# Performance work log

Hardware: AMD Instinct MI355X
Metric: run time of the kernel (lower is better)

## Reference

```python
import jax, jax.numpy as jnp
import numpy as np

D_MODEL = 1024
N_HEADS = 16
HEAD_DIM = D_MODEL // N_HEADS
B, T = 4, 2048
EPS = 1e-5


def _layernorm(x, w, b):
    mu = jnp.mean(x, axis=-1, keepdims=True)
    var = jnp.mean(jnp.square(x - mu), axis=-1, keepdims=True)
    return (x - mu) * jax.lax.rsqrt(var + EPS) * w + b


def _heads(x, w, b):
    # x: [B,T,D]; w stored [in,out] so y = x @ w + b (== torch Linear)
    y = x @ w + b
    return y.reshape(B, T, N_HEADS, HEAD_DIM).transpose(0, 2, 1, 3)  # [B,H,T,hd]


def _attention(q, k, v):
    scores = jnp.einsum('bhqd,bhkd->bhqk', q, k) / np.sqrt(HEAD_DIM).astype(np.float32)
    attn = jax.nn.softmax(scores, axis=-1)  # dropout is identity in eval mode
    o = jnp.einsum('bhqk,bhkd->bhqd', attn, v)
    return o.transpose(0, 2, 1, 3).reshape(B, T, D_MODEL)


def setup_inputs() -> dict:
    key = jax.random.key(0)
    ks = jax.random.split(key, 16)
    s = 1.0 / np.sqrt(D_MODEL)
    def lin(k, din, dout):
        kw, kb = jax.random.split(k)
        return (jax.random.uniform(kw, (din, dout), jnp.float32, -s, s),
                jax.random.uniform(kb, (dout,), jnp.float32, -s, s))
    inp = {}
    inp['temporal_tokens'] = jax.random.normal(ks[0], (B, T, D_MODEL), jnp.float32)
    inp['feature_tokens'] = jax.random.normal(ks[1], (B, T, D_MODEL), jnp.float32)
    names = ['qt', 'kf', 'vf', 'qf', 'kt', 'vt', 'ot', 'of']
    for i, n in enumerate(names):
        w, b = lin(ks[2 + i], D_MODEL, D_MODEL)
        inp[n + '_w'], inp[n + '_b'] = w, b
    inp['fus1_w'], inp['fus1_b'] = lin(ks[10], 2 * D_MODEL, D_MODEL)
    inp['fus2_w'], inp['fus2_b'] = lin(ks[11], D_MODEL, D_MODEL)
    for n in ['ln_fus', 'ln_t', 'ln_f']:
        inp[n + '_w'] = jnp.ones((D_MODEL,), jnp.float32)
        inp[n + '_b'] = jnp.zeros((D_MODEL,), jnp.float32)
    return inp


def reference(temporal_tokens, feature_tokens,
              qt_w, qt_b, kf_w, kf_b, vf_w, vf_b,
              qf_w, qf_b, kt_w, kt_b, vt_w, vt_b,
              ot_w, ot_b, of_w, of_b,
              fus1_w, fus1_b, fus2_w, fus2_b,
              ln_fus_w, ln_fus_b, ln_t_w, ln_t_b, ln_f_w, ln_f_b):
    # temporal -> feature cross attention
    Qt = _heads(temporal_tokens, qt_w, qt_b)
    Kf = _heads(feature_tokens, kf_w, kf_b)
    Vf = _heads(feature_tokens, vf_w, vf_b)
    attn_t = _attention(Qt, Kf, Vf) @ ot_w + ot_b
    fused_t = _layernorm(temporal_tokens + attn_t, ln_t_w, ln_t_b)
    # feature -> temporal cross attention
    Qf = _heads(feature_tokens, qf_w, qf_b)
    Kt = _heads(temporal_tokens, kt_w, kt_b)
    Vt = _heads(temporal_tokens, vt_w, vt_b)
    attn_f = _attention(Qf, Kt, Vt) @ of_w + of_b
    fused_f = _layernorm(feature_tokens + attn_f, ln_f_w, ln_f_b)
    # fusion MLP
    combined = jnp.concatenate([fused_t, fused_f], axis=-1)  # [B,T,2D]
    h = jax.nn.gelu(combined @ fus1_w + fus1_b, approximate=False)
    fused = _layernorm(h @ fus2_w + fus2_b, ln_fus_w, ln_fus_b)
    return fused
```

## Files before the change

### kernel.cpp

```cpp
#include <hip/hip_runtime.h>
#include <math.h>

typedef __attribute__((ext_vector_type(8))) short short8;
typedef __attribute__((ext_vector_type(4))) short short4v;
typedef __attribute__((ext_vector_type(4))) float floatx4;
typedef __attribute__((ext_vector_type(16))) float floatx16;

#define GLOBAL_AS __attribute__((address_space(1)))
#define LDS_AS __attribute__((address_space(3)))

__device__ __forceinline__ float bf2f(unsigned short u) {
    unsigned int x = ((unsigned int)u) << 16;
    return __builtin_bit_cast(float, x);
}
__device__ __forceinline__ unsigned short f2bf(float f) {
    unsigned int u = __builtin_bit_cast(unsigned int, f);
    u += 0x7fffu + ((u >> 16) & 1u);
    return (unsigned short)(u >> 16);
}

struct WX {
    const float* src[10];
    unsigned long long dst[10];
    int r64[10];
    int cum[11];
};

__global__ __launch_bounds__(256) void prep_kernel(
    WX P, unsigned short* __restrict__ base,
    const float* __restrict__ ta, const float* __restrict__ tb,
    unsigned short* __restrict__ oa, unsigned short* __restrict__ ob)
{
    __shared__ unsigned short T[64][72];
    const int bx = blockIdx.x;
    if (bx >= P.cum[10]) {
        const int cb = bx - P.cum[10];
        const float* in = cb < 1024 ? ta : tb;
        unsigned short* out = cb < 1024 ? oa : ob;
        const size_t b0 = (size_t)(cb & 1023) * 8192;
        #pragma unroll
        for (int j = 0; j < 8; ++j) {
            const size_t i = b0 + (size_t)j * 1024 + threadIdx.x * 4;
            float4 f = *(const float4*)(in + i);
            unsigned short o[4] = {f2bf(f.x), f2bf(f.y), f2bf(f.z), f2bf(f.w)};
            *(uint2*)(out + i) = *(const uint2*)o;
        }
        return;
    }
    int w = 0;
    #pragma unroll
    for (int i = 0; i < 10; ++i) if (bx >= P.cum[i + 1]) w = i + 1;
    const int tix = bx - P.cum[w];
    const int R = P.r64[w] * 64;
    const int r0 = (tix >> 4) * 64, c0 = (tix & 15) * 64;
    const float* in = P.src[w];
    unsigned short* out = base + P.dst[w];
    const int t = threadIdx.x;
    {
        const int r = t >> 2, cc = (t & 3) * 16;
        const float* p = in + (size_t)(r0 + r) * 1024 + c0 + cc;
        #pragma unroll
        for (int j = 0; j < 16; j += 4) {
            float4 f = *(const float4*)(p + j);
            T[cc + j + 0][r] = f2bf(f.x);
            T[cc + j + 1][r] = f2bf(f.y);
            T[cc + j + 2][r] = f2bf(f.z);
            T[cc + j + 3][r] = f2bf(f.w);
        }
    }
    __syncthreads();
    {
        const int c = t >> 2, rr = (t & 3) * 16;
        unsigned short* q = out + (size_t)(c0 + c) * R + r0 + rr;
        *(uint4*)(q)     = *(const uint4*)(&T[c][rr]);
        *(uint4*)(q + 8) = *(const uint4*)(&T[c][rr + 8]);
    }
}

#define GEMM_CORE(A_, B_, Kdim)                                               \
    const int tid = threadIdx.x;                                              \
    const int wave = tid >> 6, lane = tid & 63;                               \
    const int l32 = lane & 31, hi = lane >> 5;                                \
    const int wm = (wave & 1) * 64, wn = (wave >> 1) * 64;                    \
    const int srow8 = lane >> 3, c8 = lane & 7;                               \
    const int scol = (c8 ^ srow8) * 8;                                        \
    floatx16 acc[2][2];                                                       \
    _Pragma("unroll")                                                         \
    for (int i = 0; i < 2; ++i)                                               \
        _Pragma("unroll")                                                     \
        for (int j = 0; j < 2; ++j)                                           \
            _Pragma("unroll")                                                 \
            for (int r = 0; r < 16; ++r) acc[i][j][r] = 0.f;                  \
    const unsigned short* pa[4];                                              \
    const unsigned short* pb[4];                                              \
    _Pragma("unroll")                                                         \
    for (int i = 0; i < 4; ++i) {                                             \
        pa[i] = (A_) + (size_t)(bm + i * 32 + wave * 8 + srow8) * (Kdim) + scol; \
        pb[i] = (B_) + (size_t)(bn + i * 32 + wave * 8 + srow8) * (Kdim) + scol; \
    }                                                                         \
    int aoff[2][4], boff[2][4];                                               \
    _Pragma("unroll")                                                         \
    for (int f = 0; f < 2; ++f)                                               \
        _Pragma("unroll")                                                     \
        for (int s = 0; s < 4; ++s) {                                         \
            const int cg = ((s * 2 + hi) ^ (l32 & 7)) * 8;                    \
            aoff[f][s] = (wm + f * 32 + l32) * 64 + cg;                       \
            boff[f][s] = (wn + f * 32 + l32) * 64 + cg;                       \
        }                                                                     \
    for (int k0 = 0; k0 < (Kdim); k0 += 64) {                                 \
        _Pragma("unroll")                                                     \
        for (int i = 0; i < 4; ++i) {                                         \
            __builtin_amdgcn_global_load_lds((const GLOBAL_AS void*)(pa[i] + k0), \
                (LDS_AS void*)(As + i * 2048 + wave * 512), 16, 0, 0);        \
            __builtin_amdgcn_global_load_lds((const GLOBAL_AS void*)(pb[i] + k0), \
                (LDS_AS void*)(Bs + i * 2048 + wave * 512), 16, 0, 0);        \
        }                                                                     \
        __syncthreads();                                                      \
        _Pragma("unroll")                                                     \
        for (int s = 0; s < 4; ++s) {                                         \
            short8 af[2], bf[2];                                              \
            _Pragma("unroll")                                                 \
            for (int f = 0; f < 2; ++f) {                                     \
                af[f] = *(const short8*)&As[aoff[f][s]];                      \
                bf[f] = *(const short8*)&Bs[boff[f][s]];                      \
            }                                                                 \
            _Pragma("unroll")                                                 \
            for (int mi = 0; mi < 2; ++mi)                                    \
                _Pragma("unroll")                                             \
                for (int ni = 0; ni < 2; ++ni)                                \
                    acc[mi][ni] = __builtin_amdgcn_mfma_f32_32x32x16_bf16(    \
                        bf[ni], af[mi], acc[mi][ni], 0, 0, 0);                \
        }                                                                     \
        __syncthreads();                                                      \
    }

template <int MODE>
__global__ __launch_bounds__(256) void gemm_kernel(
    const unsigned short* __restrict__ A,
    const unsigned short* __restrict__ Wt,
    const float* __restrict__ bias,
    unsigned short* __restrict__ C,
    int N, int K)
{
    __shared__ unsigned short As[128 * 64];
    __shared__ unsigned short Bs[128 * 64];
    const int bm = blockIdx.x * 128, bn = blockIdx.y * 128;
    GEMM_CORE(A, Wt, K)

    #pragma unroll
    for (int mi = 0; mi < 2; ++mi) {
        const int m = bm + wm + mi * 32 + l32;
        #pragma unroll
        for (int ni = 0; ni < 2; ++ni) {
            #pragma unroll
            for (int rg = 0; rg < 4; ++rg) {
                const int n0 = bn + wn + ni * 32 + rg * 8 + hi * 4;
                float4 bv = *(const float4*)&bias[n0];
                float v[4];
                #pragma unroll
                for (int r = 0; r < 4; ++r)
                    v[r] = acc[mi][ni][rg * 4 + r] + ((const float*)&bv)[r];
                if (MODE == 2) {
                    #pragma unroll
                    for (int r = 0; r < 4; ++r)
                        v[r] = 0.5f * v[r] * (1.0f + erff(v[r] * 0.70710678118f));
                }
                unsigned short o[4] = {f2bf(v[0]), f2bf(v[1]), f2bf(v[2]), f2bf(v[3])};
                *(uint2*)&C[(size_t)m * N + n0] = *(const uint2*)o;
            }
        }
    }
}

__global__ __launch_bounds__(256) void gemm_out_kernel(
    const unsigned short* __restrict__ A0, const unsigned short* __restrict__ W0,
    const float* __restrict__ bi0, const float* __restrict__ r0, unsigned short* __restrict__ C0,
    const unsigned short* __restrict__ A1, const unsigned short* __restrict__ W1,
    const float* __restrict__ bi1, const float* __restrict__ r1, unsigned short* __restrict__ C1)
{
    __shared__ unsigned short As[128 * 64];
    __shared__ unsigned short Bs[128 * 64];
    const int s1 = blockIdx.y >> 3;
    const unsigned short* A = s1 ? A1 : A0;
    const unsigned short* Wt = s1 ? W1 : W0;
    const float* bias = s1 ? bi1 : bi0;
    const float* resid = s1 ? r1 : r0;
    unsigned short* C = s1 ? C1 : C0;
    const int bm = blockIdx.x * 128, bn = (blockIdx.y & 7) * 128;
    GEMM_CORE(A, Wt, 1024)

    #pragma unroll
    for (int mi = 0; mi < 2; ++mi) {
        const int m = bm + wm + mi * 32 + l32;
        #pragma unroll
        for (int ni = 0; ni < 2; ++ni) {
            #pragma unroll
            for (int rg = 0; rg < 4; ++rg) {
                const int n0 = bn + wn + ni * 32 + rg * 8 + hi * 4;
                float4 bv = *(const float4*)&bias[n0];
                float4 rv = *(const float4*)&resid[(size_t)m * 1024 + n0];
                float v[4];
                v[0] = acc[mi][ni][rg * 4 + 0] + bv.x + rv.x;
                v[1] = acc[mi][ni][rg * 4 + 1] + bv.y + rv.y;
                v[2] = acc[mi][ni][rg * 4 + 2] + bv.z + rv.z;
                v[3] = acc[mi][ni][rg * 4 + 3] + bv.w + rv.w;
                unsigned short o[4] = {f2bf(v[0]), f2bf(v[1]), f2bf(v[2]), f2bf(v[3])};
                *(uint2*)&C[(size_t)m * 1024 + n0] = *(const uint2*)o;
            }
        }
    }
}

__global__ __launch_bounds__(256) void gemm_qkv_kernel(
    const unsigned short* __restrict__ At, const unsigned short* __restrict__ Wt3t,
    const float* __restrict__ tb0, const float* __restrict__ tb1, const float* __restrict__ tb2,
    unsigned short* __restrict__ to0, unsigned short* __restrict__ to1, unsigned short* __restrict__ to2,
    const unsigned short* __restrict__ Af, const unsigned short* __restrict__ Wt3f,
    const float* __restrict__ fb0, const float* __restrict__ fb1, const float* __restrict__ fb2,
    unsigned short* __restrict__ fo0, unsigned short* __restrict__ fo1, unsigned short* __restrict__ fo2,
    float scale0)
{
    __shared__ unsigned short As[128 * 64];
    __shared__ unsigned short Bs[128 * 64];
    const int str = blockIdx.y >= 24;
    const unsigned short* A = str ? Af : At;
    const unsigned short* Wt = str ? Wt3f : Wt3t;
    const int byy = str ? (blockIdx.y - 24) : blockIdx.y;
    const int buf = byy >> 3;
    const int bn = byy * 128;
    const int cn = (byy & 7) * 128;
    const float* bias = str ? (buf == 0 ? fb0 : (buf == 1 ? fb1 : fb2))
                            : (buf == 0 ? tb0 : (buf == 1 ? tb1 : tb2));
    unsigned short* C = str ? (buf == 0 ? fo0 : (buf == 1 ? fo1 : fo2))
                            : (buf == 0 ? to0 : (buf == 1 ? to1 : to2));
    const float scale = buf == 0 ? scale0 : 1.0f;
    const int bm = blockIdx.x * 128;
    GEMM_CORE(A, Wt, 1024)

    #pragma unroll
    for (int mi = 0; mi < 2; ++mi) {
        const int m = bm + wm + mi * 32 + l32;
        #pragma unroll
        for (int ni = 0; ni < 2; ++ni) {
            #pragma unroll
            for (int rg = 0; rg < 4; ++rg) {
                const int n0 = cn + wn + ni * 32 + rg * 8 + hi * 4;
                float4 bv = *(const float4*)&bias[n0];
                unsigned short o[4];
                #pragma unroll
                for (int r = 0; r < 4; ++r)
                    o[r] = f2bf((acc[mi][ni][rg * 4 + r] + ((const float*)&bv)[r]) * scale);
                if (buf == 2) {
                    const int b = m >> 11, t = m & 2047;
                    const int h = n0 >> 6, d0 = n0 & 63;
                    const int tsw = t ^ ((d0 & 8) ? 4 : 0);
                    unsigned short* vb = C + ((size_t)(b * 16 + h) * 64) * 2048 + tsw;
                    #pragma unroll
                    for (int r = 0; r < 4; ++r) vb[(size_t)(d0 + r) * 2048] = o[r];
                } else {
                    *(uint2*)&C[(size_t)m * 1024 + n0] = *(const uint2*)o;
                }
            }
        }
    }
}

__global__ __launch_bounds__(256) void flash_kernel(
    const unsigned short* __restrict__ Q0, const unsigned short* __restrict__ K0,
    const unsigned short* __restrict__ V0, unsigned short* __restrict__ O0,
    const unsigned short* __restrict__ Q1, const unsigned short* __restrict__ K1,
    const unsigned short* __restrict__ V1, unsigned short* __restrict__ O1)
{
    __shared__ unsigned short Ks[64 * 64];
    __shared__ unsigned short Vs[64 * 64];

    const int bid = blockIdx.x;
    const int p = (bid & 7) * 16 + (bid >> 7);
    const int qt = (bid >> 3) & 15;
    const int s1 = p >= 64;
    const int rem = p & 63;
    const int b = rem >> 4, h = rem & 15;
    const unsigned short* Q = s1 ? Q1 : Q0;
    const unsigned short* Kmat = s1 ? K1 : K0;
    const unsigned short* Vtp = s1 ? V1 : V0;
    unsigned short* O = s1 ? O1 : O0;
    const int q0 = qt * 128;

    const int tid = threadIdx.x;
    const int wave = tid >> 6, lane = tid & 63;
    const int quad = lane >> 4, l16 = lane & 15;

    const unsigned short* qp = Q + (size_t)(b * 2048 + q0 + wave * 32 + l16) * 1024 + h * 64;
    short8 qf[2][2];
    qf[0][0] = *(const short8*)(qp + quad * 8);
    qf[0][1] = *(const short8*)(qp + 32 + quad * 8);
    qf[1][0] = *(const short8*)(qp + 16 * 1024 + quad * 8);
    qf[1][1] = *(const short8*)(qp + 16 * 1024 + 32 + quad * 8);

    const int srow8 = lane >> 3;
    const int c8 = lane & 7;
    const int rit0 = wave * 16 + srow8;
    const int rit1 = rit0 + 8;
    const int col0 = (c8 ^ (rit0 & 7)) * 8;
    const int col1 = (c8 ^ (rit1 & 7)) * 8;
    const unsigned short* kbase = Kmat + (size_t)b * 2048 * 1024 + h * 64;
    const unsigned short* vbase = Vtp + (size_t)(b * 16 + h) * 64 * 2048;
    unsigned short* lk0 = Ks + (wave * 16) * 64;
    unsigned short* lk1 = lk0 + 8 * 64;
    unsigned short* lv0 = Vs + (wave * 16) * 64;
    unsigned short* lv1 = lv0 + 8 * 64;

    int koff[4][2];
    #pragma unroll
    for (int nt = 0; nt < 4; ++nt)
        #pragma unroll
        for (int hh = 0; hh < 2; ++hh)
            koff[nt][hh] = (nt * 16 + l16) * 64 + (((hh * 4 + quad) ^ (l16 & 7)) * 8);
    int voff[4][4];
    #pragma unroll
    for (int dt = 0; dt < 4; ++dt)
        #pragma unroll
        for (int nt = 0; nt < 4; ++nt)
            voff[dt][nt] = (dt * 16 + l16) * 64 +
                           (((nt * 2 + (quad >> 1)) ^ (l16 & 7)) * 8) +
                           (((quad & 1) ^ (l16 >> 3)) * 4);

    floatx4 oa[2][4], la[2];
    #pragma unroll
    for (int qg = 0; qg < 2; ++qg) {
        la[qg] = (floatx4){0.f, 0.f, 0.f, 0.f};
        #pragma unroll
        for (int dt = 0; dt < 4; ++dt) oa[qg][dt] = (floatx4){0.f, 0.f, 0.f, 0.f};
    }
    const short4v vone = {(short)0x3F80, (short)0x3F80, (short)0x3F80, (short)0x3F80};

    for (int kt = 0; kt < 32; ++kt) {
        const unsigned short* kg0 = kbase + (size_t)(kt * 64 + rit0) * 1024 + col0;
        const unsigned short* kg1 = kbase + (size_t)(kt * 64 + rit1) * 1024 + col1;
        const unsigned short* vg0 = vbase + (size_t)rit0 * 2048 + kt * 64 + col0;
        const unsigned short* vg1 = vbase + (size_t)rit1 * 2048 + kt * 64 + col1;
        __builtin_amdgcn_global_load_lds((const GLOBAL_AS void*)kg0, (LDS_AS void*)lk0, 16, 0, 0);
        __builtin_amdgcn_global_load_lds((const GLOBAL_AS void*)kg1, (LDS_AS void*)lk1, 16, 0, 0);
        __builtin_amdgcn_global_load_lds((const GLOBAL_AS void*)vg0, (LDS_AS void*)lv0, 16, 0, 0);
        __builtin_amdgcn_global_load_lds((const GLOBAL_AS void*)vg1, (LDS_AS void*)lv1, 16, 0, 0);
        __syncthreads();

        short4v pf[2][4];
        #pragma unroll
        for (int nt = 0; nt < 4; ++nt) {
            short8 k0 = *(const short8*)&Ks[koff[nt][0]];
            short8 k1 = *(const short8*)&Ks[koff[nt][1]];
            #pragma unroll
            for (int qg = 0; qg < 2; ++qg) {
                floatx4 s = (floatx4){0.f, 0.f, 0.f, 0.f};
                s = __builtin_amdgcn_mfma_f32_16x16x32_bf16(k0, qf[qg][0], s, 0, 0, 0);
                s = __builtin_amdgcn_mfma_f32_16x16x32_bf16(k1, qf[qg][1], s, 0, 0, 0);
                float p0 = __builtin_amdgcn_exp2f(s[0]);
                float p1 = __builtin_amdgcn_exp2f(s[1]);
                float p2 = __builtin_amdgcn_exp2f(s[2]);
                float p3 = __builtin_amdgcn_exp2f(s[3]);
                unsigned u0 = __builtin_bit_cast(unsigned, p0) + 0x8000u;
                unsigned u1 = __builtin_bit_cast(unsigned, p1) + 0x8000u;
                unsigned u2 = __builtin_bit_cast(unsigned, p2) + 0x8000u;
                unsigned u3 = __builtin_bit_cast(unsigned, p3) + 0x8000u;
                union { unsigned u[2]; short4v s4; } pk;
                pk.u[0] = __builtin_amdgcn_perm(u1, u0, 0x07060302u);
                pk.u[1] = __builtin_amdgcn_perm(u3, u2, 0x07060302u);
                pf[qg][nt] = pk.s4;
                la[qg] = __builtin_amdgcn_mfma_f32_16x16x16bf16_1k(vone, pf[qg][nt], la[qg], 0, 0, 0);
            }
        }
        #pragma unroll
        for (int dt = 0; dt < 4; ++dt)
            #pragma unroll
            for (int nt = 0; nt < 4; ++nt) {
                short4v vf = *(const short4v*)&Vs[voff[dt][nt]];
                oa[0][dt] = __builtin_amdgcn_mfma_f32_16x16x16bf16_1k(vf, pf[0][nt], oa[0][dt], 0, 0, 0);
                oa[1][dt] = __builtin_amdgcn_mfma_f32_16x16x16bf16_1k(vf, pf[1][nt], oa[1][dt], 0, 0, 0);
            }
        __syncthreads();
    }

    #pragma unroll
    for (int qg = 0; qg < 2; ++qg) {
        const float linv = 1.0f / la[qg][0];
        unsigned short* orow = O + (size_t)(b * 2048 + q0 + wave * 32 + qg * 16 + l16) * 1024 + h * 64;
        #pragma unroll
        for (int dt = 0; dt < 4; ++dt) {
            unsigned short ob[4];
            #pragma unroll
            for (int r = 0; r < 4; ++r) ob[r] = f2bf(oa[qg][dt][r] * linv);
            *(uint2*)(orow + dt * 16 + quad * 4) = *(const uint2*)ob;
        }
    }
}

__global__ __launch_bounds__(256) void ln2_kernel(
    const unsigned short* __restrict__ in0, const unsigned short* __restrict__ in1,
    unsigned short* __restrict__ out,
    const float* __restrict__ w0, const float* __restrict__ b0,
    const float* __restrict__ w1, const float* __restrict__ b1)
{
    __shared__ float red[8];
    const int sel = blockIdx.x >> 13;
    const int row = blockIdx.x & 8191;
    const unsigned short* in = sel ? in1 : in0;
    const float* w = sel ? w1 : w0;
    const float* bb = sel ? b1 : b0;
    const int tid = threadIdx.x;
    const int wave = tid >> 6, lane = tid & 63;
    uint2 raw = *(const uint2*)(in + (size_t)row * 1024 + tid * 4);
    float v[4];
    v[0] = bf2f((unsigned short)(raw.x & 0xffffu));
    v[1] = bf2f((unsigned short)(raw.x >> 16));
    v[2] = bf2f((unsigned short)(raw.y & 0xffffu));
    v[3] = bf2f((unsigned short)(raw.y >> 16));
    float s = v[0] + v[1] + v[2] + v[3];
    float sq = v[0] * v[0] + v[1] * v[1] + v[2] * v[2] + v[3] * v[3];
    #pragma unroll
    for (int m = 1; m < 64; m <<= 1) { s += __shfl_xor(s, m); sq += __shfl_xor(sq, m); }
    if (lane == 0) { red[wave] = s; red[4 + wave] = sq; }
    __syncthreads();
    s = red[0] + red[1] + red[2] + red[3];
    sq = red[4] + red[5] + red[6] + red[7];
    const float mu = s * (1.0f / 1024.0f);
    const float var = sq * (1.0f / 1024.0f) - mu * mu;
    const float rstd = rsqrtf(var + 1e-5f);
    unsigned short ob[4];
    #pragma unroll
    for (int j = 0; j < 4; ++j)
        ob[j] = f2bf((v[j] - mu) * rstd * w[tid * 4 + j] + bb[tid * 4 + j]);
    *(uint2*)(out + (size_t)row * 2048 + sel * 1024 + tid * 4) = *(uint2*)ob;
}

__global__ __launch_bounds__(256) void ln_final_kernel(
    const unsigned short* __restrict__ in, float* __restrict__ out,
    const float* __restrict__ w, const float* __restrict__ bias)
{
    __shared__ float red[8];
    const int row = blockIdx.x;
    const int tid = threadIdx.x;
    const int wave = tid >> 6, lane = tid & 63;
    uint2 raw = *(const uint2*)(in + (size_t)row * 1024 + tid * 4);
    float v[4];
    v[0] = bf2f((unsigned short)(raw.x & 0xffffu));
    v[1] = bf2f((unsigned short)(raw.x >> 16));
    v[2] = bf2f((unsigned short)(raw.y & 0xffffu));
    v[3] = bf2f((unsigned short)(raw.y >> 16));
    float s = v[0] + v[1] + v[2] + v[3];
    float sq = v[0] * v[0] + v[1] * v[1] + v[2] * v[2] + v[3] * v[3];
    #pragma unroll
    for (int m = 1; m < 64; m <<= 1) { s += __shfl_xor(s, m); sq += __shfl_xor(sq, m); }
    if (lane == 0) { red[wave] = s; red[4 + wave] = sq; }
    __syncthreads();
    s = red[0] + red[1] + red[2] + red[3];
    sq = red[4] + red[5] + red[6] + red[7];
    const float mu = s * (1.0f / 1024.0f);
    const float var = sq * (1.0f / 1024.0f) - mu * mu;
    const float rstd = rsqrtf(var + 1e-5f);
    float o[4];
    #pragma unroll
    for (int j = 0; j < 4; ++j)
        o[j] = (v[j] - mu) * rstd * w[tid * 4 + j] + bias[tid * 4 + j];
    *(float4*)(out + (size_t)row * 1024 + tid * 4) = (float4){o[0], o[1], o[2], o[3]};
}

extern "C" void kernel_launch(void* const* d_in, const int* in_sizes, int n_in,
                              void* d_out, int out_size, void* d_ws, size_t ws_size,
                              hipStream_t stream)
{
    (void)in_sizes; (void)n_in; (void)out_size; (void)ws_size;
    const float* temporal = (const float*)d_in[0];
    const float* feature  = (const float*)d_in[1];
    const float* qt_w = (const float*)d_in[2];
    const float* qt_b = (const float*)d_in[3];
    const float* kf_w = (const float*)d_in[4];
    const float* kf_b = (const float*)d_in[5];
    const float* vf_w = (const float*)d_in[6];
    const float* vf_b = (const float*)d_in[7];
    const float* qf_w = (const float*)d_in[8];
    const float* qf_b = (const float*)d_in[9];
    const float* kt_w = (const float*)d_in[10];
    const float* kt_b = (const float*)d_in[11];
    const float* vt_w = (const float*)d_in[12];
    const float* vt_b = (const float*)d_in[13];
    const float* ot_w = (const float*)d_in[14];
    const float* ot_b = (const float*)d_in[15];
    const float* of_w = (const float*)d_in[16];
    const float* of_b = (const float*)d_in[17];
    const float* fus1_w = (const float*)d_in[18];
    const float* fus1_b = (const float*)d_in[19];
    const float* fus2_w = (const float*)d_in[20];
    const float* fus2_b = (const float*)d_in[21];
    const float* ln_fus_w = (const float*)d_in[22];
    const float* ln_fus_b = (const float*)d_in[23];
    const float* ln_t_w = (const float*)d_in[24];
    const float* ln_t_b = (const float*)d_in[25];
    const float* ln_f_w = (const float*)d_in[26];
    const float* ln_f_b = (const float*)d_in[27];

    unsigned short* p = (unsigned short*)d_ws;
    const size_t EW = 1024ull * 1024;
    const size_t ET = 8192ull * 1024;
    unsigned short* WT3t = p;
    unsigned short* WT3f = p + 3 * EW;
    unsigned short* WTot = p + 6 * EW;
    unsigned short* WTof = p + 7 * EW;
    unsigned short* WTf1 = p + 8 * EW;
    unsigned short* WTf2 = p + 10 * EW;
    size_t off = 11 * EW;
    unsigned short* Tb = p + off; off += ET;
    unsigned short* Fb = p + off; off += ET;
    unsigned short* Qt = p + off; off += ET;
    unsigned short* Kt = p + off; off += ET;
    unsigned short* Vt = p + off; off += ET;
    unsigned short* Qf = p + off; off += ET;
    unsigned short* Kf = p + off; off += ET;
    unsigned short* Vf = p + off; off += ET;
    unsigned short* VfT = p + off; off += ET;
    unsigned short* VtT = p + off; off += ET;
    unsigned short* attnT = p + off; off += ET;
    unsigned short* attnF = p + off; off += ET;
    unsigned short* yT = Qt;
    unsigned short* yF = Qf;
    unsigned short* comb = Kt;
    unsigned short* hbuf = Kf;
    unsigned short* y2 = Vf;
    (void)Vt;

    const float SC = 0.125f * 1.4426950408889634f;

    {
        WX P;
        const float* srcs[10] = {qt_w, kt_w, vt_w, qf_w, kf_w, vf_w,
                                 ot_w, of_w, fus1_w, fus2_w};
        unsigned long long dsts[10] = {
            0, EW, 2 * EW,
            3 * EW, 4 * EW, 5 * EW,
            6 * EW, 7 * EW, 8 * EW, 10 * EW};
        int cum = 0;
        P.cum[0] = 0;
        for (int i = 0; i < 10; ++i) {
            P.src[i] = srcs[i];
            P.dst[i] = dsts[i];
            P.r64[i] = (i == 8) ? 32 : 16;
            cum += P.r64[i] * 16;
            P.cum[i + 1] = cum;
        }
        prep_kernel<<<cum + 2048, 256, 0, stream>>>(P, p, temporal, feature, Tb, Fb);
    }

    const dim3 gb(256);
    gemm_qkv_kernel<<<dim3(64, 48), gb, 0, stream>>>(
        Tb, WT3t, qt_b, kt_b, vt_b, Qt, Kt, VtT,
        Fb, WT3f, qf_b, kf_b, vf_b, Qf, Kf, VfT, SC);
    flash_kernel<<<2048, gb, 0, stream>>>(
        Qt, Kf, VfT, attnT, Qf, Kt, VtT, attnF);
    gemm_out_kernel<<<dim3(64, 16), gb, 0, stream>>>(
        attnT, WTot, ot_b, temporal, yT,
        attnF, WTof, of_b, feature,  yF);
    ln2_kernel<<<16384, gb, 0, stream>>>(yT, yF, comb, ln_t_w, ln_t_b, ln_f_w, ln_f_b);
    gemm_kernel<2><<<dim3(64, 8), gb, 0, stream>>>(comb, WTf1, fus1_b, hbuf, 1024, 2048);
    gemm_kernel<0><<<dim3(64, 8), gb, 0, stream>>>(hbuf, WTf2, fus2_b, y2, 1024, 1024);
    ln_final_kernel<<<8192, gb, 0, stream>>>(y2, (float*)d_out, ln_fus_w, ln_fus_b);
}
```

Measured before the change: 655.6 us.

## Double-buffer K/V tiles in flash attention kernel to overlap loads with compute

The flash attention loop now uses two LDS buffers for K and V tiles. The next tile's global-to-LDS load is issued before computing on the current tile, with an explicit vmcnt wait and barrier between stages. It also raises wave priority around the PV MFMA block. The goal is to hide global load latency behind MFMA work, at the cost of doubling LDS use (32KB per block), which may reduce occupancy.

```diff
diff --git a/kernel.cpp b/kernel.cpp
--- a/kernel.cpp
+++ b/kernel.cpp
@@ -271,8 +271,8 @@
     const unsigned short* __restrict__ Q1, const unsigned short* __restrict__ K1,
     const unsigned short* __restrict__ V1, unsigned short* __restrict__ O1)
 {
-    __shared__ unsigned short Ks[64 * 64];
-    __shared__ unsigned short Vs[64 * 64];
+    __shared__ unsigned short Ks[2 * 64 * 64];
+    __shared__ unsigned short Vs[2 * 64 * 64];
 
     const int bid = blockIdx.x;
     const int p = (bid & 7) * 16 + (bid >> 7);
@@ -334,52 +334,84 @@
     }
     const short4v vone = {(short)0x3F80, (short)0x3F80, (short)0x3F80, (short)0x3F80};
 
-    for (int kt = 0; kt < 32; ++kt) {
-        const unsigned short* kg0 = kbase + (size_t)(kt * 64 + rit0) * 1024 + col0;
-        const unsigned short* kg1 = kbase + (size_t)(kt * 64 + rit1) * 1024 + col1;
-        const unsigned short* vg0 = vbase + (size_t)rit0 * 2048 + kt * 64 + col0;
-        const unsigned short* vg1 = vbase + (size_t)rit1 * 2048 + kt * 64 + col1;
-        __builtin_amdgcn_global_load_lds((const GLOBAL_AS void*)kg0, (LDS_AS void*)lk0, 16, 0, 0);
-        __builtin_amdgcn_global_load_lds((const GLOBAL_AS void*)kg1, (LDS_AS void*)lk1, 16, 0, 0);
-        __builtin_amdgcn_global_load_lds((const GLOBAL_AS void*)vg0, (LDS_AS void*)lv0, 16, 0, 0);
-        __builtin_amdgcn_global_load_lds((const GLOBAL_AS void*)vg1, (LDS_AS void*)lv1, 16, 0, 0);
-        __syncthreads();
-
-        short4v pf[2][4];
-        #pragma unroll
-        for (int nt = 0; nt < 4; ++nt) {
-            short8 k0 = *(const short8*)&Ks[koff[nt][0]];
-            short8 k1 = *(const short8*)&Ks[koff[nt][1]];
-            #pragma unroll
-            for (int qg = 0; qg < 2; ++qg) {
-                floatx4 s = (floatx4){0.f, 0.f, 0.f, 0.f};
-                s = __builtin_amdgcn_mfma_f32_16x16x32_bf16(k0, qf[qg][0], s, 0, 0, 0);
-                s = __builtin_amdgcn_mfma_f32_16x16x32_bf16(k1, qf[qg][1], s, 0, 0, 0);
-                float p0 = __builtin_amdgcn_exp2f(s[0]);
-                float p1 = __builtin_amdgcn_exp2f(s[1]);
-                float p2 = __builtin_amdgcn_exp2f(s[2]);
-                float p3 = __builtin_amdgcn_exp2f(s[3]);
-                unsigned u0 = __builtin_bit_cast(unsigned, p0) + 0x8000u;
-                unsigned u1 = __builtin_bit_cast(unsigned, p1) + 0x8000u;
-                unsigned u2 = __builtin_bit_cast(unsigned, p2) + 0x8000u;
-                unsigned u3 = __builtin_bit_cast(unsigned, p3) + 0x8000u;
-                union { unsigned u[2]; short4v s4; } pk;
-                pk.u[0] = __builtin_amdgcn_perm(u1, u0, 0x07060302u);
-                pk.u[1] = __builtin_amdgcn_perm(u3, u2, 0x07060302u);
-                pf[qg][nt] = pk.s4;
-                la[qg] = __builtin_amdgcn_mfma_f32_16x16x16bf16_1k(vone, pf[qg][nt], la[qg], 0, 0, 0);
-            }
-        }
-        #pragma unroll
-        for (int dt = 0; dt < 4; ++dt)
-            #pragma unroll
-            for (int nt = 0; nt < 4; ++nt) {
-                short4v vf = *(const short4v*)&Vs[voff[dt][nt]];
-                oa[0][dt] = __builtin_amdgcn_mfma_f32_16x16x16bf16_1k(vf, pf[0][nt], oa[0][dt], 0, 0, 0);
-                oa[1][dt] = __builtin_amdgcn_mfma_f32_16x16x16bf16_1k(vf, pf[1][nt], oa[1][dt], 0, 0, 0);
-            }
-        __syncthreads();
-    }
+    const unsigned short* kg0p = kbase + (size_t)rit0 * 1024 + col0;
+    const unsigned short* kg1p = kbase + (size_t)rit1 * 1024 + col1;
+    const unsigned short* vg0p = vbase + (size_t)rit0 * 2048 + col0;
+    const unsigned short* vg1p = vbase + (size_t)rit1 * 2048 + col1;
+
+#define FLASH_STAGE(BO) do {                                                   \
+        __builtin_amdgcn_global_load_lds((const GLOBAL_AS void*)kg0p,          \
+            (LDS_AS void*)(lk0 + (BO)), 16, 0, 0);                             \
+        __builtin_amdgcn_global_load_lds((const GLOBAL_AS void*)kg1p,          \
+            (LDS_AS void*)(lk1 + (BO)), 16, 0, 0);                             \
+        __builtin_amdgcn_global_load_lds((const GLOBAL_AS void*)vg0p,          \
+            (LDS_AS void*)(lv0 + (BO)), 16, 0, 0);                             \
+        __builtin_amdgcn_global_load_lds((const GLOBAL_AS void*)vg1p,          \
+            (LDS_AS void*)(lv1 + (BO)), 16, 0, 0);                             \
+        kg0p += 64 * 1024; kg1p += 64 * 1024; vg0p += 64; vg1p += 64;          \
+    } while (0)
+
+#define FLASH_SYNC() do {                                                      \
+        asm volatile("s_waitcnt vmcnt(0)" ::: "memory");                       \
+        __builtin_amdgcn_s_barrier();                                          \
+    } while (0)
+
+#define FLASH_COMPUTE(BO) do {                                                 \
+        short4v pf[2][4];                                                      \
+        _Pragma("unroll")                                                      \
+        for (int nt = 0; nt < 4; ++nt) {                                       \
+            short8 k0 = *(const short8*)&Ks[(BO) + koff[nt][0]];               \
+            short8 k1 = *(const short8*)&Ks[(BO) + koff[nt][1]];               \
+            _Pragma("unroll")                                                  \
+            for (int qg = 0; qg < 2; ++qg) {                                   \
+                floatx4 sv = (floatx4){0.f, 0.f, 0.f, 0.f};                    \
+                sv = __builtin_amdgcn_mfma_f32_16x16x32_bf16(k0, qf[qg][0], sv, 0, 0, 0); \
+                sv = __builtin_amdgcn_mfma_f32_16x16x32_bf16(k1, qf[qg][1], sv, 0, 0, 0); \
+                float p0 = __builtin_amdgcn_exp2f(sv[0]);                      \
+                float p1 = __builtin_amdgcn_exp2f(sv[1]);                      \
+                float p2 = __builtin_amdgcn_exp2f(sv[2]);                      \
+                float p3 = __builtin_amdgcn_exp2f(sv[3]);                      \
+                unsigned u0 = __builtin_bit_cast(unsigned, p0) + 0x8000u;      \
+                unsigned u1 = __builtin_bit_cast(unsigned, p1) + 0x8000u;      \
+                unsigned u2 = __builtin_bit_cast(unsigned, p2) + 0x8000u;      \
+                unsigned u3 = __builtin_bit_cast(unsigned, p3) + 0x8000u;      \
+                union { unsigned u[2]; short4v s4; } pk;                       \
+                pk.u[0] = __builtin_amdgcn_perm(u1, u0, 0x07060302u);          \
+                pk.u[1] = __builtin_amdgcn_perm(u3, u2, 0x07060302u);          \
+                pf[qg][nt] = pk.s4;                                            \
+                la[qg] = __builtin_amdgcn_mfma_f32_16x16x16bf16_1k(vone, pf[qg][nt], la[qg], 0, 0, 0); \
+            }                                                                  \
+        }                                                                      \
+        __builtin_amdgcn_s_setprio(1);                                         \
+        _Pragma("unroll")                                                      \
+        for (int dt = 0; dt < 4; ++dt)                                         \
+            _Pragma("unroll")                                                  \
+            for (int nt = 0; nt < 4; ++nt) {                                   \
+                short4v vf = *(const short4v*)&Vs[(BO) + voff[dt][nt]];        \
+                oa[0][dt] = __builtin_amdgcn_mfma_f32_16x16x16bf16_1k(vf, pf[0][nt], oa[0][dt], 0, 0, 0); \
+                oa[1][dt] = __builtin_amdgcn_mfma_f32_16x16x16bf16_1k(vf, pf[1][nt], oa[1][dt], 0, 0, 0); \
+            }                                                                  \
+        __builtin_amdgcn_s_setprio(0);                                         \
+    } while (0)
+
+    FLASH_STAGE(0);
+    FLASH_SYNC();
+    for (int kt = 0; kt < 30; kt += 2) {
+        FLASH_STAGE(4096);
+        FLASH_COMPUTE(0);
+        FLASH_SYNC();
+        FLASH_STAGE(0);
+        FLASH_COMPUTE(4096);
+        FLASH_SYNC();
+    }
+    FLASH_STAGE(4096);
+    FLASH_COMPUTE(0);
+    FLASH_SYNC();
+    FLASH_COMPUTE(4096);
+
+#undef FLASH_STAGE
+#undef FLASH_SYNC
+#undef FLASH_COMPUTE
 
     #pragma unroll
     for (int qg = 0; qg < 2; ++qg) {
```

After: 657.6 us. About the same (+0.3%).
